# Optimization experiments

Measured on AMD Instinct MI355X. Metric: run time of the kernel, lower is better.

## Reference

```python
import jax, jax.numpy as jnp
import numpy as np

B, L, D = 2, 2048, 1024
H = 16          # num_heads == num_key_value_heads
FD = 16         # feature_dim (q/k head dim)
HD = D // H     # head_dim = 64 (v head dim)
EPS = 1e-5


def setup_inputs() -> dict:
    key = jax.random.key(0)
    k0, k1, k2, k3, k4 = jax.random.split(key, 5)
    scale = 0.02
    return {
        "hidden_states": jax.random.normal(k0, (B, L, D), jnp.float32),
        "Wq": jax.random.normal(k1, (D, H * FD), jnp.float32) * scale,
        "Wk": jax.random.normal(k2, (D, H * FD), jnp.float32) * scale,
        "Wv": jax.random.normal(k3, (D, H * HD), jnp.float32) * scale,
        "Wo": jax.random.normal(k4, (H * HD, D), jnp.float32) * scale,
    }


def reference(hidden_states, Wq, Wk, Wv, Wo):
    # projections (bias-free), split heads: b l (h d) -> b h l d
    q = (hidden_states @ Wq).reshape(B, L, H, FD).transpose(0, 2, 1, 3)
    k = (hidden_states @ Wk).reshape(B, L, H, FD).transpose(0, 2, 1, 3)
    v = (hidden_states @ Wv).reshape(B, L, H, HD).transpose(0, 2, 1, 3)

    # parallel_rebased: squared-dot-product kernel attention, causal,
    # row-normalized by the kernel sum (use_scale=True, use_normalize=True)
    qk_scale = FD ** -0.5
    s = jnp.einsum('bhqd,bhkd->bhqk', q * qk_scale, k)
    s = s * s  # quadratic feature map: (q.k)^2
    causal = jnp.tril(jnp.ones((L, L), dtype=bool))
    s = jnp.where(causal, s, 0.0)
    z = jnp.sum(s, axis=-1)  # [B,H,L]
    o = jnp.einsum('bhqk,bhkd->bhqd', s, v) / (z[..., None] + EPS)

    # merge heads: b h l d -> b l (h d), output projection
    o = o.transpose(0, 2, 1, 3).reshape(B, L, H * HD)
    return o @ Wo
```

## Files before the change

### kernel.cpp

```cpp
#include <hip/hip_runtime.h>
#include <hip/hip_bf16.h>

#define BB 2
#define LL 2048
#define DD 1024
#define HH 16
#define FD 16
#define HD 64
#define EPS 1e-5f
#define RQKV 1536
#define NFIX 4

typedef __attribute__((ext_vector_type(4))) float f32x4;
typedef __attribute__((ext_vector_type(8))) _Float16 f16x8;
typedef __attribute__((ext_vector_type(4))) _Float16 f16x4;

__global__ __launch_bounds__(256) void prep(
    const float* __restrict__ Wq, const float* __restrict__ Wk,
    const float* __restrict__ Wv, const float* __restrict__ Wo,
    const float* __restrict__ hs, _Float16* __restrict__ WqkvT,
    _Float16* __restrict__ WoT, float* __restrict__ QKVe,
    _Float16* __restrict__ HS16) {
  __shared__ __attribute__((aligned(16))) char smem[40960];
  const int bx = blockIdx.x;
  const int tid = threadIdx.x;

  if (bx >= 2608) {
    int idx = ((bx - 2608) * 256 + tid) * 16;
#pragma unroll
    for (int half = 0; half < 2; half++) {
      float4 a = *(const float4*)(hs + idx + half * 8);
      float4 b = *(const float4*)(hs + idx + half * 8 + 4);
      f16x8 p = {(_Float16)a.x, (_Float16)a.y, (_Float16)a.z, (_Float16)a.w,
                 (_Float16)b.x, (_Float16)b.y, (_Float16)b.z, (_Float16)b.w};
      *(f16x8*)(HS16 + idx + half * 8) = p;
    }
    return;
  }

  if (bx < 2560) {
    _Float16(*s)[40] = (_Float16(*)[40])smem;
    const float* src;
    _Float16* dst;
    int n0, ncol, drow, k0;
    if (bx < 1536) {
      int ct = bx % 48, kt = bx / 48;
      if (ct < 8) { src = Wq; n0 = ct * 32; ncol = 256; drow = n0; }
      else if (ct < 16) { src = Wk; n0 = (ct - 8) * 32; ncol = 256; drow = 256 + n0; }
      else { src = Wv; n0 = (ct - 16) * 32; ncol = 1024; drow = 512 + n0; }
      k0 = kt * 32;
      dst = WqkvT;
    } else {
      int i2 = bx - 1536;
      n0 = (i2 & 31) * 32; k0 = (i2 >> 5) * 32;
      src = Wo; ncol = DD; drow = n0; dst = WoT;
    }
    {
      int r = tid >> 3, c = (tid & 7) * 4;
      float4 v = *(const float4*)(src + (size_t)(k0 + r) * ncol + n0 + c);
      f16x4 p = {(_Float16)v.x, (_Float16)v.y, (_Float16)v.z, (_Float16)v.w};
      *(f16x4*)&s[r][c] = p;
    }
    __syncthreads();
    {
      int n = tid >> 3, kk = (tid & 7) * 4;
      f16x4 o = {s[kk + 0][n], s[kk + 1][n], s[kk + 2][n], s[kk + 3][n]};
      *(f16x4*)(dst + (size_t)(drow + n) * DD + k0 + kk) = o;
    }
    return;
  }

  float(*sHS)[DD] = (float(*)[DD])smem;
  float(*part)[8][32] = (float(*)[8][32])(smem + 32768);
  const int kg = tid >> 5, c = tid & 31;
  const int c0 = (bx - 2560) * 32;

  for (int i = tid; i < 8 * (DD / 4); i += 256) {
    int e = i / (DD / 4), col4 = (i % (DD / 4)) * 4;
    int b = e >> 2, r = e & 3;
    *(float4*)&sHS[e][col4] =
        *(const float4*)(hs + (size_t)(b * LL + r) * DD + col4);
  }
  __syncthreads();

  const float* W;
  int col, ncol;
  if (c0 < 256) { W = Wq; col = c0 + c; ncol = 256; }
  else if (c0 < 512) { W = Wk; col = (c0 - 256) + c; ncol = 256; }
  else { W = Wv; col = (c0 - 512) + c; ncol = 1024; }

  float acc[8] = {};
  const int d0 = kg * 128;
#pragma unroll 4
  for (int d = d0; d < d0 + 128; d++) {
    float wv = W[(size_t)d * ncol + col];
#pragma unroll
    for (int e = 0; e < 8; e++) acc[e] += sHS[e][d] * wv;
  }
#pragma unroll
  for (int e = 0; e < 8; e++) part[kg][e][c] = acc[e];
  __syncthreads();

  {
    int e = tid >> 5;
    float t = 0.f;
#pragma unroll
    for (int g = 0; g < 8; g++) t += part[g][e][c];
    QKVe[(size_t)e * RQKV + c0 + c] = t;
  }
}

template <typename OutT>
__global__ __launch_bounds__(256) void gemm_f16(
    const _Float16* __restrict__ A, const _Float16* __restrict__ Bt,
    OutT* __restrict__ C, int M, int N, int K) {
  __shared__ __attribute__((aligned(16))) _Float16 sA[128 * 64];
  __shared__ __attribute__((aligned(16))) _Float16 sB[64 * 64];
  const int tid = threadIdx.x;
  const int m0 = blockIdx.y * 128, n0 = blockIdx.x * 64;
  const int w = tid >> 6, lane = tid & 63, quad = lane >> 4, l16 = lane & 15;
  const int wm = (w >> 1) * 64, wn = (w & 1) * 32;

  const int sr = tid >> 1, p = tid & 1;
  const int brow = (tid & 127) >> 1;
  const _Float16* Ag = A + (size_t)(m0 + sr) * K + p * 32;
  const _Float16* Bg = Bt + (size_t)(n0 + brow) * K + p * 32;
  _Float16* sAw = &sA[sr * 64];
  _Float16* sBw = &sB[brow * 64];
  const int aswz = sr & 7, bswz = brow & 7;

  f32x4 acc[4][2];
#pragma unroll
  for (int i = 0; i < 4; i++)
#pragma unroll
    for (int j = 0; j < 2; j++) acc[i][j] = (f32x4){0.f, 0.f, 0.f, 0.f};

  f16x8 ar[4], br[4];
  auto LOAD = [&](int k0) {
#pragma unroll
    for (int i = 0; i < 4; i++) ar[i] = *(const f16x8*)(Ag + k0 + i * 8);
    if (tid < 128) {
#pragma unroll
      for (int i = 0; i < 4; i++) br[i] = *(const f16x8*)(Bg + k0 + i * 8);
    }
  };
  LOAD(0);

  for (int k0 = 0; k0 < K; k0 += 64) {
    __syncthreads();
#pragma unroll
    for (int i = 0; i < 4; i++)
      *(f16x8*)(sAw + (((4 * p + i) ^ aswz) * 8)) = ar[i];
    if (tid < 128) {
#pragma unroll
      for (int i = 0; i < 4; i++)
        *(f16x8*)(sBw + (((4 * p + i) ^ bswz) * 8)) = br[i];
    }
    __syncthreads();
    if (k0 + 64 < K) LOAD(k0 + 64);

#pragma unroll
    for (int s = 0; s < 2; s++) {
      f16x8 af[4], bf[2];
#pragma unroll
      for (int i = 0; i < 4; i++) {
        int row = wm + i * 16 + l16;
        int col = ((s * 4 + quad) ^ (row & 7)) * 8;
        af[i] = *(const f16x8*)&sA[row * 64 + col];
      }
#pragma unroll
      for (int j = 0; j < 2; j++) {
        int row = wn + j * 16 + l16;
        int col = ((s * 4 + quad) ^ (row & 7)) * 8;
        bf[j] = *(const f16x8*)&sB[row * 64 + col];
      }
#pragma unroll
      for (int i = 0; i < 4; i++)
#pragma unroll
        for (int j = 0; j < 2; j++)
          acc[i][j] = __builtin_amdgcn_mfma_f32_16x16x32_f16(af[i], bf[j], acc[i][j], 0, 0, 0);
    }
  }

#pragma unroll
  for (int i = 0; i < 4; i++)
#pragma unroll
    for (int j = 0; j < 2; j++)
#pragma unroll
      for (int r = 0; r < 4; r++) {
        const int row = m0 + wm + i * 16 + quad * 4 + r;
        const int col = n0 + wn + j * 16 + l16;
        C[(size_t)row * N + col] = (OutT)acc[i][j][r];
      }
}

#define SK4 24
#define SV4 88
#define SS4 88

__global__ __launch_bounds__(256) void attn_mfma4(
    const _Float16* __restrict__ QKV, _Float16* __restrict__ O) {
  __shared__ __attribute__((aligned(16))) _Float16 sK[64 * SK4];
  __shared__ __attribute__((aligned(16))) _Float16 sVt[80 * SV4];
  __shared__ __attribute__((aligned(16))) _Float16 sS2[4 * 32 * SS4];

  const int bh = blockIdx.x;
  const int b = bh >> 4, h = bh & 15;
  const int qtA = blockIdx.y;
  const int qtB = 31 - qtA;
  const int tid = threadIdx.x;
  const int w = tid >> 6;
  const int lane = tid & 63;
  const int quad = lane >> 4;
  const int l16 = lane & 15;
  const int gqA = qtA * 64 + w * 16;
  const int gqB = qtB * 64 + w * 16;

  f16x8 qfragA = {}, qfragB = {};
  if (quad < 2) {
    qfragA = *(const f16x8*)(QKV +
        (size_t)(b * LL + gqA + l16) * RQKV + h * FD + quad * 8);
    qfragB = *(const f16x8*)(QKV +
        (size_t)(b * LL + gqB + l16) * RQKV + h * FD + quad * 8);
    const _Float16 RT2 = (_Float16)1.41421356f;
#pragma unroll
    for (int i = 0; i < 8; i++) {
      qfragA[i] = qfragA[i] * RT2;
      qfragB[i] = qfragB[i] * RT2;
    }
  }

  for (int t = tid; t < 16 * SV4; t += 256) {
    int r = t / SV4, c = t % SV4;
    sVt[64 * SV4 + t] = (_Float16)((r == 0 && c < 64) ? 1.0f : 0.0f);
  }
  __syncthreads();
  const f16x8 zf0 = *(const f16x8*)&sVt[(64 + l16) * SV4 + quad * 8];
  const f16x8 zf1 = *(const f16x8*)&sVt[(64 + l16) * SV4 + 32 + quad * 8];

  f32x4 oaccA[4], oaccB[4];
  f32x4 zaccA = (f32x4){0.f, 0.f, 0.f, 0.f};
  f32x4 zaccB = (f32x4){0.f, 0.f, 0.f, 0.f};
#pragma unroll
  for (int nt = 0; nt < 4; nt++) {
    oaccA[nt] = (f32x4){0.f, 0.f, 0.f, 0.f};
    oaccB[nt] = (f32x4){0.f, 0.f, 0.f, 0.f};
  }

  _Float16* sS2B = sS2 + w * 32 * SS4;
  _Float16* sS2A = sS2B + 16 * SS4;

  const int ktiles = qtB + 1;

  const int skey = tid >> 2, sfg = (tid & 3) * 4;
  uint2 kreg;
  f16x8 vreg0, vreg1;
  auto LOAD = [&](int kt) {
    kreg = *(const uint2*)(QKV +
        (size_t)(b * LL + kt * 64 + skey) * RQKV + 256 + h * FD + sfg);
    const _Float16* vp = QKV +
        (size_t)(b * LL + kt * 64 + lane) * RQKV + 512 + h * HD + w * 16;
    vreg0 = *(const f16x8*)vp;
    vreg1 = *(const f16x8*)(vp + 8);
  };
  LOAD(0);

  for (int kt = 0; kt < ktiles; kt++) {
    __syncthreads();
    *(uint2*)&sK[skey * SK4 + sfg] = kreg;
#pragma unroll
    for (int t = 0; t < 8; t++) sVt[(w * 16 + t) * SV4 + lane] = vreg0[t];
#pragma unroll
    for (int t = 0; t < 8; t++) sVt[(w * 16 + 8 + t) * SV4 + lane] = vreg1[t];
    __syncthreads();
    if (kt + 1 < ktiles) LOAD(kt + 1);

    const int k0 = kt * 64;
    const bool activeA = (kt <= qtA);

    f16x8 kf[4];
#pragma unroll
    for (int nt = 0; nt < 4; nt++) {
      f16x8 f = {};
      if (quad < 2) f = *(const f16x8*)&sK[(nt * 16 + l16) * SK4 + quad * 8];
      kf[nt] = f;
    }

    {
      const bool mask = (kt == qtB);
#pragma unroll
      for (int nt = 0; nt < 4; nt++) {
        f32x4 s = __builtin_amdgcn_mfma_f32_16x16x32_f16(
            qfragB, kf[nt], (f32x4){0.f, 0.f, 0.f, 0.f}, 0, 0, 0);
        const int gk = k0 + nt * 16 + l16;
#pragma unroll
        for (int r = 0; r < 4; r++) {
          float sv = s[r] * s[r];
          if (mask) sv = (gk <= gqB + quad * 4 + r) ? sv : 0.0f;
          sS2B[(quad * 4 + r) * SS4 + nt * 16 + l16] = (_Float16)sv;
        }
      }
    }
    if (activeA) {
      const bool mask = (kt == qtA);
#pragma unroll
      for (int nt = 0; nt < 4; nt++) {
        f32x4 s = __builtin_amdgcn_mfma_f32_16x16x32_f16(
            qfragA, kf[nt], (f32x4){0.f, 0.f, 0.f, 0.f}, 0, 0, 0);
        const int gk = k0 + nt * 16 + l16;
#pragma unroll
        for (int r = 0; r < 4; r++) {
          float sv = s[r] * s[r];
          if (mask) sv = (gk <= gqA + quad * 4 + r) ? sv : 0.0f;
          sS2A[(quad * 4 + r) * SS4 + nt * 16 + l16] = (_Float16)sv;
        }
      }
    }
    __asm__ volatile("s_waitcnt lgkmcnt(0)" ::: "memory");

    f16x8 afB0 = *(const f16x8*)&sS2B[l16 * SS4 + quad * 8];
    f16x8 afB1 = *(const f16x8*)&sS2B[l16 * SS4 + 32 + quad * 8];
    f16x8 afA0 = {}, afA1 = {};
    if (activeA) {
      afA0 = *(const f16x8*)&sS2A[l16 * SS4 + quad * 8];
      afA1 = *(const f16x8*)&sS2A[l16 * SS4 + 32 + quad * 8];
    }

#pragma unroll
    for (int nt = 0; nt < 4; nt++) {
      f16x8 vf0 = *(const f16x8*)&sVt[(nt * 16 + l16) * SV4 + quad * 8];
      f16x8 vf1 = *(const f16x8*)&sVt[(nt * 16 + l16) * SV4 + 32 + quad * 8];
      oaccB[nt] = __builtin_amdgcn_mfma_f32_16x16x32_f16(afB0, vf0, oaccB[nt], 0, 0, 0);
      oaccB[nt] = __builtin_amdgcn_mfma_f32_16x16x32_f16(afB1, vf1, oaccB[nt], 0, 0, 0);
      if (activeA) {
        oaccA[nt] = __builtin_amdgcn_mfma_f32_16x16x32_f16(afA0, vf0, oaccA[nt], 0, 0, 0);
        oaccA[nt] = __builtin_amdgcn_mfma_f32_16x16x32_f16(afA1, vf1, oaccA[nt], 0, 0, 0);
      }
    }
    zaccB = __builtin_amdgcn_mfma_f32_16x16x32_f16(afB0, zf0, zaccB, 0, 0, 0);
    zaccB = __builtin_amdgcn_mfma_f32_16x16x32_f16(afB1, zf1, zaccB, 0, 0, 0);
    if (activeA) {
      zaccA = __builtin_amdgcn_mfma_f32_16x16x32_f16(afA0, zf0, zaccA, 0, 0, 0);
      zaccA = __builtin_amdgcn_mfma_f32_16x16x32_f16(afA1, zf1, zaccA, 0, 0, 0);
    }
  }

  {
    float rz[4];
#pragma unroll
    for (int r = 0; r < 4; r++) {
      float zz = __shfl(zaccB[r], lane & 48);
      rz[r] = 1.0f / (zz + 32.0f * EPS);
    }
#pragma unroll
    for (int nt = 0; nt < 4; nt++)
#pragma unroll
      for (int r = 0; r < 4; r++) {
        const int gq = gqB + quad * 4 + r;
        O[(size_t)(b * LL + gq) * (HH * HD) + h * HD + nt * 16 + l16] =
            (_Float16)(oaccB[nt][r] * rz[r]);
      }
  }
  {
    float rz[4];
#pragma unroll
    for (int r = 0; r < 4; r++) {
      float zz = __shfl(zaccA[r], lane & 48);
      rz[r] = 1.0f / (zz + 32.0f * EPS);
    }
#pragma unroll
    for (int nt = 0; nt < 4; nt++)
#pragma unroll
      for (int r = 0; r < 4; r++) {
        const int gq = gqA + quad * 4 + r;
        O[(size_t)(b * LL + gq) * (HH * HD) + h * HD + nt * 16 + l16] =
            (_Float16)(oaccA[nt][r] * rz[r]);
      }
  }
}

__global__ __launch_bounds__(256) void fix_final(
    const float* __restrict__ QKVe, _Float16* __restrict__ Oatt) {
  const int b = blockIdx.x >> 4, h = blockIdx.x & 15;
  const int tid = threadIdx.x;
  const int p = tid >> 6, d = tid & 63;

  float num = 0.f, z = 0.f;
  const float* qrow = QKVe + (size_t)(b * 4 + p) * RQKV + h * FD;
  for (int j = 0; j <= p; j++) {
    const float* krow = QKVe + (size_t)(b * 4 + j) * RQKV + 256 + h * FD;
    float s = 0.f;
#pragma unroll
    for (int f = 0; f < FD; f++) s += qrow[f] * krow[f];
    s *= 0.25f;
    s = s * s;
    z += s;
    num += s * QKVe[(size_t)(b * 4 + j) * RQKV + 512 + h * HD + d];
  }
  Oatt[(size_t)(b * LL + p) * (HH * HD) + h * HD + d] =
      (_Float16)(num / (z + EPS));
}

extern "C" void kernel_launch(void* const* d_in, const int* in_sizes, int n_in,
                              void* d_out, int out_size, void* d_ws, size_t ws_size,
                              hipStream_t stream) {
  const float* hs = (const float*)d_in[0];
  const float* Wq = (const float*)d_in[1];
  const float* Wk = (const float*)d_in[2];
  const float* Wv = (const float*)d_in[3];
  const float* Wo = (const float*)d_in[4];
  float* out = (float*)d_out;

  char* ws = (char*)d_ws;
  _Float16* WqkvT = (_Float16*)ws;
  _Float16* WoT   = (_Float16*)(ws + (3ull << 20));
  _Float16* HS16  = (_Float16*)(ws + (5ull << 20));
  _Float16* QKV   = (_Float16*)(ws + (13ull << 20));
  _Float16* Oatt  = (_Float16*)(ws + (25ull << 20));
  float*    QKVe  = (float*)(ws + (33ull << 20));

  const int M = BB * LL;

  prep<<<dim3(3632), 256, 0, stream>>>(Wq, Wk, Wv, Wo, hs, WqkvT, WoT, QKVe, HS16);

  gemm_f16<_Float16><<<dim3(RQKV / 64, M / 128), 256, 0, stream>>>(
      HS16, WqkvT, QKV, M, RQKV, DD);

  attn_mfma4<<<dim3(BB * HH, LL / 128), 256, 0, stream>>>(QKV, Oatt);

  fix_final<<<dim3(BB * HH), 256, 0, stream>>>(QKVe, Oatt);

  gemm_f16<float><<<dim3(DD / 64, M / 128), 256, 0, stream>>>(
      Oatt, WoT, out, M, DD, DD);
}
```

Baseline: 172.4 us.

## Replace paired-query-tile attention blocks with one tile per block and 128-key staging

The attention kernel no longer pairs a short and a long query tile in one block for causal load balancing. Each block now handles a single 64-row query tile, so the grid doubles, and blocks are launched longest-first by reversing blockIdx.y. Keys and values are staged in 128-key chunks, which halves the number of barrier and load iterations per tile. Register use drops because only one set of accumulators is kept, and a launch-bounds hint asks for 4 blocks per CU. The risk is less even work per block, with a causal tail left to hardware scheduling, plus extra LDS use for the wider V buffer.

```diff
diff --git a/kernel.cpp b/kernel.cpp
--- a/kernel.cpp
+++ b/kernel.cpp
@@ -194,154 +194,125 @@
       }
 }
 
-#define SK4 24
-#define SV4 88
-#define SS4 88
-
-__global__ __launch_bounds__(256) void attn_mfma4(
+#define SK5 24
+#define SV5 136
+#define SS5 88
+
+__global__ __launch_bounds__(256, 4) void attn_mfma5(
     const _Float16* __restrict__ QKV, _Float16* __restrict__ O) {
-  __shared__ __attribute__((aligned(16))) _Float16 sK[64 * SK4];
-  __shared__ __attribute__((aligned(16))) _Float16 sVt[80 * SV4];
-  __shared__ __attribute__((aligned(16))) _Float16 sS2[4 * 32 * SS4];
+  __shared__ __attribute__((aligned(16))) _Float16 sK[128 * SK5];
+  __shared__ __attribute__((aligned(16))) _Float16 sVt[80 * SV5];
+  __shared__ __attribute__((aligned(16))) _Float16 sS2[4 * 16 * SS5];
 
   const int bh = blockIdx.x;
   const int b = bh >> 4, h = bh & 15;
-  const int qtA = blockIdx.y;
-  const int qtB = 31 - qtA;
+  const int qt = 31 - blockIdx.y;
   const int tid = threadIdx.x;
   const int w = tid >> 6;
   const int lane = tid & 63;
   const int quad = lane >> 4;
   const int l16 = lane & 15;
-  const int gqA = qtA * 64 + w * 16;
-  const int gqB = qtB * 64 + w * 16;
-
-  f16x8 qfragA = {}, qfragB = {};
+  const int gq = qt * 64 + w * 16;
+
+  f16x8 qfrag = {};
   if (quad < 2) {
-    qfragA = *(const f16x8*)(QKV +
-        (size_t)(b * LL + gqA + l16) * RQKV + h * FD + quad * 8);
-    qfragB = *(const f16x8*)(QKV +
-        (size_t)(b * LL + gqB + l16) * RQKV + h * FD + quad * 8);
+    qfrag = *(const f16x8*)(QKV +
+        (size_t)(b * LL + gq + l16) * RQKV + h * FD + quad * 8);
     const _Float16 RT2 = (_Float16)1.41421356f;
 #pragma unroll
-    for (int i = 0; i < 8; i++) {
-      qfragA[i] = qfragA[i] * RT2;
-      qfragB[i] = qfragB[i] * RT2;
-    }
-  }
-
-  for (int t = tid; t < 16 * SV4; t += 256) {
-    int r = t / SV4, c = t % SV4;
-    sVt[64 * SV4 + t] = (_Float16)((r == 0 && c < 64) ? 1.0f : 0.0f);
+    for (int i = 0; i < 8; i++) qfrag[i] = qfrag[i] * RT2;
+  }
+
+  for (int t = tid; t < 16 * SV5; t += 256) {
+    int r = t / SV5, c = t % SV5;
+    sVt[64 * SV5 + t] = (_Float16)((r == 0 && c < 128) ? 1.0f : 0.0f);
   }
   __syncthreads();
-  const f16x8 zf0 = *(const f16x8*)&sVt[(64 + l16) * SV4 + quad * 8];
-  const f16x8 zf1 = *(const f16x8*)&sVt[(64 + l16) * SV4 + 32 + quad * 8];
-
-  f32x4 oaccA[4], oaccB[4];
-  f32x4 zaccA = (f32x4){0.f, 0.f, 0.f, 0.f};
-  f32x4 zaccB = (f32x4){0.f, 0.f, 0.f, 0.f};
-#pragma unroll
-  for (int nt = 0; nt < 4; nt++) {
-    oaccA[nt] = (f32x4){0.f, 0.f, 0.f, 0.f};
-    oaccB[nt] = (f32x4){0.f, 0.f, 0.f, 0.f};
-  }
-
-  _Float16* sS2B = sS2 + w * 32 * SS4;
-  _Float16* sS2A = sS2B + 16 * SS4;
-
-  const int ktiles = qtB + 1;
-
-  const int skey = tid >> 2, sfg = (tid & 3) * 4;
-  uint2 kreg;
-  f16x8 vreg0, vreg1;
+  const f16x8 zf0 = *(const f16x8*)&sVt[(64 + l16) * SV5 + quad * 8];
+  const f16x8 zf1 = *(const f16x8*)&sVt[(64 + l16) * SV5 + 32 + quad * 8];
+
+  f32x4 oacc[4];
+  f32x4 zacc = (f32x4){0.f, 0.f, 0.f, 0.f};
+#pragma unroll
+  for (int nt = 0; nt < 4; nt++) oacc[nt] = (f32x4){0.f, 0.f, 0.f, 0.f};
+
+  _Float16* sS2w = sS2 + w * 16 * SS5;
+
+  const int nst = qt + 1;
+  const int nkt = (nst + 1) >> 1;
+
+  const int krow = tid >> 1, kcol = (tid & 1) * 8;
+  f16x8 kreg;
+  f16x8 vreg0, vreg1, vreg2, vreg3;
   auto LOAD = [&](int kt) {
-    kreg = *(const uint2*)(QKV +
-        (size_t)(b * LL + kt * 64 + skey) * RQKV + 256 + h * FD + sfg);
+    kreg = *(const f16x8*)(QKV +
+        (size_t)(b * LL + kt * 128 + krow) * RQKV + 256 + h * FD + kcol);
     const _Float16* vp = QKV +
-        (size_t)(b * LL + kt * 64 + lane) * RQKV + 512 + h * HD + w * 16;
+        (size_t)(b * LL + kt * 128 + lane) * RQKV + 512 + h * HD + w * 16;
     vreg0 = *(const f16x8*)vp;
     vreg1 = *(const f16x8*)(vp + 8);
+    vp += (size_t)64 * RQKV;
+    vreg2 = *(const f16x8*)vp;
+    vreg3 = *(const f16x8*)(vp + 8);
   };
   LOAD(0);
 
-  for (int kt = 0; kt < ktiles; kt++) {
-    __syncthreads();
-    *(uint2*)&sK[skey * SK4 + sfg] = kreg;
-#pragma unroll
-    for (int t = 0; t < 8; t++) sVt[(w * 16 + t) * SV4 + lane] = vreg0[t];
-#pragma unroll
-    for (int t = 0; t < 8; t++) sVt[(w * 16 + 8 + t) * SV4 + lane] = vreg1[t];
-    __syncthreads();
-    if (kt + 1 < ktiles) LOAD(kt + 1);
-
-    const int k0 = kt * 64;
-    const bool activeA = (kt <= qtA);
-
-    f16x8 kf[4];
-#pragma unroll
-    for (int nt = 0; nt < 4; nt++) {
-      f16x8 f = {};
-      if (quad < 2) f = *(const f16x8*)&sK[(nt * 16 + l16) * SK4 + quad * 8];
-      kf[nt] = f;
-    }
-
-    {
-      const bool mask = (kt == qtB);
+  for (int kt = 0; kt < nkt; kt++) {
+    __syncthreads();
+    *(f16x8*)&sK[krow * SK5 + kcol] = kreg;
+#pragma unroll
+    for (int t = 0; t < 8; t++) sVt[(w * 16 + t) * SV5 + lane] = vreg0[t];
+#pragma unroll
+    for (int t = 0; t < 8; t++) sVt[(w * 16 + 8 + t) * SV5 + lane] = vreg1[t];
+#pragma unroll
+    for (int t = 0; t < 8; t++) sVt[(w * 16 + t) * SV5 + 64 + lane] = vreg2[t];
+#pragma unroll
+    for (int t = 0; t < 8; t++) sVt[(w * 16 + 8 + t) * SV5 + 64 + lane] = vreg3[t];
+    __syncthreads();
+    if (kt + 1 < nkt) LOAD(kt + 1);
+
+#pragma unroll
+    for (int hf = 0; hf < 2; hf++) {
+      const int st = 2 * kt + hf;
+      if (st >= nst) break;
+      const int k0 = st * 64;
+      const bool mask = (st == qt);
+
+      f16x8 kf[4];
+#pragma unroll
+      for (int nt = 0; nt < 4; nt++) {
+        f16x8 f = {};
+        if (quad < 2)
+          f = *(const f16x8*)&sK[(hf * 64 + nt * 16 + l16) * SK5 + quad * 8];
+        kf[nt] = f;
+      }
+
 #pragma unroll
       for (int nt = 0; nt < 4; nt++) {
         f32x4 s = __builtin_amdgcn_mfma_f32_16x16x32_f16(
-            qfragB, kf[nt], (f32x4){0.f, 0.f, 0.f, 0.f}, 0, 0, 0);
+            qfrag, kf[nt], (f32x4){0.f, 0.f, 0.f, 0.f}, 0, 0, 0);
         const int gk = k0 + nt * 16 + l16;
 #pragma unroll
         for (int r = 0; r < 4; r++) {
           float sv = s[r] * s[r];
-          if (mask) sv = (gk <= gqB + quad * 4 + r) ? sv : 0.0f;
-          sS2B[(quad * 4 + r) * SS4 + nt * 16 + l16] = (_Float16)sv;
+          if (mask) sv = (gk <= gq + quad * 4 + r) ? sv : 0.0f;
+          sS2w[(quad * 4 + r) * SS5 + nt * 16 + l16] = (_Float16)sv;
         }
       }
-    }
-    if (activeA) {
-      const bool mask = (kt == qtA);
+      __asm__ volatile("s_waitcnt lgkmcnt(0)" ::: "memory");
+
+      f16x8 af0 = *(const f16x8*)&sS2w[l16 * SS5 + quad * 8];
+      f16x8 af1 = *(const f16x8*)&sS2w[l16 * SS5 + 32 + quad * 8];
+
 #pragma unroll
       for (int nt = 0; nt < 4; nt++) {
-        f32x4 s = __builtin_amdgcn_mfma_f32_16x16x32_f16(
-            qfragA, kf[nt], (f32x4){0.f, 0.f, 0.f, 0.f}, 0, 0, 0);
-        const int gk = k0 + nt * 16 + l16;
-#pragma unroll
-        for (int r = 0; r < 4; r++) {
-          float sv = s[r] * s[r];
-          if (mask) sv = (gk <= gqA + quad * 4 + r) ? sv : 0.0f;
-          sS2A[(quad * 4 + r) * SS4 + nt * 16 + l16] = (_Float16)sv;
-        }
-      }
-    }
-    __asm__ volatile("s_waitcnt lgkmcnt(0)" ::: "memory");
-
-    f16x8 afB0 = *(const f16x8*)&sS2B[l16 * SS4 + quad * 8];
-    f16x8 afB1 = *(const f16x8*)&sS2B[l16 * SS4 + 32 + quad * 8];
-    f16x8 afA0 = {}, afA1 = {};
-    if (activeA) {
-      afA0 = *(const f16x8*)&sS2A[l16 * SS4 + quad * 8];
-      afA1 = *(const f16x8*)&sS2A[l16 * SS4 + 32 + quad * 8];
-    }
-
-#pragma unroll
-    for (int nt = 0; nt < 4; nt++) {
-      f16x8 vf0 = *(const f16x8*)&sVt[(nt * 16 + l16) * SV4 + quad * 8];
-      f16x8 vf1 = *(const f16x8*)&sVt[(nt * 16 + l16) * SV4 + 32 + quad * 8];
-      oaccB[nt] = __builtin_amdgcn_mfma_f32_16x16x32_f16(afB0, vf0, oaccB[nt], 0, 0, 0);
-      oaccB[nt] = __builtin_amdgcn_mfma_f32_16x16x32_f16(afB1, vf1, oaccB[nt], 0, 0, 0);
-      if (activeA) {
-        oaccA[nt] = __builtin_amdgcn_mfma_f32_16x16x32_f16(afA0, vf0, oaccA[nt], 0, 0, 0);
-        oaccA[nt] = __builtin_amdgcn_mfma_f32_16x16x32_f16(afA1, vf1, oaccA[nt], 0, 0, 0);
-      }
-    }
-    zaccB = __builtin_amdgcn_mfma_f32_16x16x32_f16(afB0, zf0, zaccB, 0, 0, 0);
-    zaccB = __builtin_amdgcn_mfma_f32_16x16x32_f16(afB1, zf1, zaccB, 0, 0, 0);
-    if (activeA) {
-      zaccA = __builtin_amdgcn_mfma_f32_16x16x32_f16(afA0, zf0, zaccA, 0, 0, 0);
-      zaccA = __builtin_amdgcn_mfma_f32_16x16x32_f16(afA1, zf1, zaccA, 0, 0, 0);
+        f16x8 vf0 = *(const f16x8*)&sVt[(nt * 16 + l16) * SV5 + hf * 64 + quad * 8];
+        f16x8 vf1 = *(const f16x8*)&sVt[(nt * 16 + l16) * SV5 + hf * 64 + 32 + quad * 8];
+        oacc[nt] = __builtin_amdgcn_mfma_f32_16x16x32_f16(af0, vf0, oacc[nt], 0, 0, 0);
+        oacc[nt] = __builtin_amdgcn_mfma_f32_16x16x32_f16(af1, vf1, oacc[nt], 0, 0, 0);
+      }
+      zacc = __builtin_amdgcn_mfma_f32_16x16x32_f16(af0, zf0, zacc, 0, 0, 0);
+      zacc = __builtin_amdgcn_mfma_f32_16x16x32_f16(af1, zf1, zacc, 0, 0, 0);
     }
   }
 
@@ -349,32 +320,16 @@
     float rz[4];
 #pragma unroll
     for (int r = 0; r < 4; r++) {
-      float zz = __shfl(zaccB[r], lane & 48);
+      float zz = __shfl(zacc[r], lane & 48);
       rz[r] = 1.0f / (zz + 32.0f * EPS);
     }
 #pragma unroll
     for (int nt = 0; nt < 4; nt++)
 #pragma unroll
       for (int r = 0; r < 4; r++) {
-        const int gq = gqB + quad * 4 + r;
-        O[(size_t)(b * LL + gq) * (HH * HD) + h * HD + nt * 16 + l16] =
-            (_Float16)(oaccB[nt][r] * rz[r]);
-      }
-  }
-  {
-    float rz[4];
-#pragma unroll
-    for (int r = 0; r < 4; r++) {
-      float zz = __shfl(zaccA[r], lane & 48);
-      rz[r] = 1.0f / (zz + 32.0f * EPS);
-    }
-#pragma unroll
-    for (int nt = 0; nt < 4; nt++)
-#pragma unroll
-      for (int r = 0; r < 4; r++) {
-        const int gq = gqA + quad * 4 + r;
-        O[(size_t)(b * LL + gq) * (HH * HD) + h * HD + nt * 16 + l16] =
-            (_Float16)(oaccA[nt][r] * rz[r]);
+        const int gqr = gq + quad * 4 + r;
+        O[(size_t)(b * LL + gqr) * (HH * HD) + h * HD + nt * 16 + l16] =
+            (_Float16)(oacc[nt][r] * rz[r]);
       }
   }
 }
@@ -426,7 +381,7 @@
   gemm_f16<_Float16><<<dim3(RQKV / 64, M / 128), 256, 0, stream>>>(
       HS16, WqkvT, QKV, M, RQKV, DD);
 
-  attn_mfma4<<<dim3(BB * HH, LL / 128), 256, 0, stream>>>(QKV, Oatt);
+  attn_mfma5<<<dim3(BB * HH, LL / 64), 256, 0, stream>>>(QKV, Oatt);
 
   fix_final<<<dim3(BB * HH), 256, 0, stream>>>(QKVe, Oatt);
 
```

New measurement: 172.9 us. Within noise of the previous version (+0.3%).
